# Kernel optimization log

Hardware: AMD Instinct MI355X
Metric: run time of the kernel (lower is better)

Reference implementation:

```python
import jax, jax.numpy as jnp
import numpy as np

N_NODES, D, H, L, E, N_DST = 100000, 64, 8, 3, 100000, 50000
HD = H * D
LEAKY_ALPHA = 0.01


def setup_inputs() -> dict:
    key = jax.random.key(0)
    ks = jax.random.split(key, 8)
    features = jax.random.normal(ks[0], (N_NODES, D), dtype=jnp.float32)
    edge_metapath_indices = jax.random.randint(ks[1], (E, L), 0, N_NODES)
    dst = jax.random.randint(ks[2], (E,), 0, N_DST)
    s = 1.0 / np.sqrt(HD)
    W_ih = jax.random.uniform(ks[3], (3 * HD, D), jnp.float32, -s, s)
    W_hh = jax.random.uniform(ks[4], (3 * HD, HD), jnp.float32, -s, s)
    b_ih = jax.random.uniform(ks[5], (3 * HD,), jnp.float32, -s, s)
    b_hh = jax.random.uniform(ks[6], (3 * HD,), jnp.float32, -s, s)
    attn = jax.random.normal(ks[7], (1, H, D), dtype=jnp.float32) * (1.414 / np.sqrt(D))
    return {"features": features, "W_ih": W_ih, "W_hh": W_hh, "b_ih": b_ih,
            "b_hh": b_hh, "attn": attn,
            "edge_metapath_indices": edge_metapath_indices, "dst": dst,
            "num_dst": N_DST}


def _gru_last_hidden(x_seq, W_ih, W_hh, b_ih, b_hh):
    # x_seq: [L, E, D]; torch nn.GRU gate math, return final hidden [E, HD]
    h0 = jnp.zeros((x_seq.shape[1], HD), dtype=x_seq.dtype)

    def step(h, x):
        gi = x @ W_ih.T + b_ih            # [E, 3HD]
        gh = h @ W_hh.T + b_hh            # [E, 3HD]
        i_r, i_z, i_n = jnp.split(gi, 3, axis=-1)
        h_r, h_z, h_n = jnp.split(gh, 3, axis=-1)
        r = jax.nn.sigmoid(i_r + h_r)
        z = jax.nn.sigmoid(i_z + h_z)
        n = jnp.tanh(i_n + r * h_n)
        h_new = (1.0 - z) * n + z * h
        return h_new, None

    h_last, _ = jax.lax.scan(step, h0, x_seq)
    return h_last


def reference(features, W_ih, W_hh, b_ih, b_hh, attn,
              edge_metapath_indices, dst, num_dst):
    # gather metapath node embeddings: [E, L, D]
    edata = features[edge_metapath_indices]
    # per-edge GRU over the metapath sequence -> final hidden [E, HD]
    hidden = _gru_last_hidden(jnp.transpose(edata, (1, 0, 2)), W_ih, W_hh, b_ih, b_hh)
    eft = hidden.reshape(-1, H, D)                         # [E, H, D]
    # attention logits per edge/head + leaky relu
    a = jnp.sum(eft * attn, axis=-1)                       # [E, H]
    a = jnp.where(a > 0, a, LEAKY_ALPHA * a)
    # edge softmax over destination-node segments (stable)
    a_max = jax.ops.segment_max(a, dst, num_segments=num_dst)    # [ND, H]
    a_exp = jnp.exp(a - a_max[dst])
    a_sum = jax.ops.segment_sum(a_exp, dst, num_segments=num_dst)
    alpha = a_exp / a_sum[dst]                             # [E, H]
    # scatter-sum aggregation of attention-weighted edge features
    ft = jax.ops.segment_sum(eft * alpha[:, :, None], dst, num_segments=num_dst)
    return ft                                              # [ND, H, D]
```

## Files before the change

### kernel.cpp

```cpp
#include <hip/hip_runtime.h>

typedef __attribute__((ext_vector_type(8))) short bf16x8;
typedef __attribute__((ext_vector_type(4))) float f32x4;

#define E_N   100000
#define ND_N  50000
#define NN_N  100000
#define SLOTS 32

__device__ __forceinline__ float b2f(unsigned short u) {
    return __uint_as_float(((unsigned int)u) << 16);
}
__device__ __forceinline__ unsigned short f2b(float f) {
    unsigned int b = __float_as_uint(f);
    b += 0x7fffu + ((b >> 16) & 1u);
    return (unsigned short)(b >> 16);
}
__device__ __forceinline__ float frcp(float x) { return __builtin_amdgcn_rcpf(x); }
__device__ __forceinline__ float fsig(float x) { return frcp(1.f + __expf(-x)); }
__device__ __forceinline__ float ftanhf(float x) {
    float e = __expf(2.f * x);
    return 1.f - 2.f * frcp(e + 1.f);
}

#define GLDS16(g, l)                                                        \
    __builtin_amdgcn_global_load_lds(                                       \
        (const __attribute__((address_space(1))) void*)(g),                 \
        (__attribute__((address_space(3))) void*)(l), 16, 0, 0)

__device__ __forceinline__ void wait_and_barrier() {
    __builtin_amdgcn_sched_barrier(0);
    asm volatile("s_waitcnt vmcnt(0)" ::: "memory");
    __builtin_amdgcn_s_barrier();
    __builtin_amdgcn_sched_barrier(0);
}
__device__ __forceinline__ void plain_barrier() {
    __builtin_amdgcn_sched_barrier(0);
    __builtin_amdgcn_s_barrier();
    __builtin_amdgcn_sched_barrier(0);
}

__global__ void conv_f2b(const float* __restrict__ src, unsigned short* __restrict__ dst, int n4) {
    int i = blockIdx.x * 256 + threadIdx.x;
    if (i < n4) {
        float4 v = ((const float4*)src)[i];
        ushort4 o;
        o.x = f2b(v.x); o.y = f2b(v.y); o.z = f2b(v.z); o.w = f2b(v.w);
        ((ushort4*)dst)[i] = o;
    }
}

__global__ void zero_u4(uint4* __restrict__ p, int n4) {
    int i = blockIdx.x * 256 + threadIdx.x;
    if (i < n4) p[i] = make_uint4(0u, 0u, 0u, 0u);
}

template<int G2>
__device__ __forceinline__ void mma_tile(
    const unsigned char* __restrict__ buf,
    f32x4 acc[4][2][2], int wm, int wn, int l15, int hi8)
{
    const unsigned char* lds_a = buf;
    const unsigned char* lds_b = buf + 16384;
    #pragma unroll
    for (int kk = 0; kk < 2; ++kk) {
        const int kb = kk * 64 + hi8 * 2;
        bf16x8 a[2];
        #pragma unroll
        for (int mi = 0; mi < 2; ++mi) {
            int row = wm * 32 + mi * 16 + l15;
            a[mi] = *(const bf16x8*)(lds_a + row * 128 + (kb ^ ((row & 7) << 4)));
        }
        #pragma unroll
        for (int g = 0; g < 3; ++g) {
            const int gi = (g == 2) ? G2 : g;
            bf16x8 b[2];
            #pragma unroll
            for (int ni = 0; ni < 2; ++ni) {
                int brow = g * 64 + wn * 32 + ni * 16 + l15;
                b[ni] = *(const bf16x8*)(lds_b + brow * 128 + (kb ^ ((brow & 7) << 4)));
            }
            #pragma unroll
            for (int mi = 0; mi < 2; ++mi)
                #pragma unroll
                for (int ni = 0; ni < 2; ++ni)
                    acc[gi][mi][ni] = __builtin_amdgcn_mfma_f32_16x16x32_bf16(
                        a[mi], b[ni], acc[gi][mi][ni], 0, 0, 0);
        }
    }
}

__global__ __launch_bounds__(512, 4) void gru_step(
    const unsigned short* __restrict__ feat16,
    const int* __restrict__ emi,
    const unsigned short* __restrict__ hprev,
    unsigned short* __restrict__ hnext,
    const unsigned short* __restrict__ wih,
    const unsigned short* __restrict__ whh,
    const float* __restrict__ bih,
    const float* __restrict__ bhh,
    int t)
{
    __shared__ __align__(16) unsigned char lds_mem[2 * 40960];

    const int tid = threadIdx.x;
    const int nwg = gridDim.x;
    const int logical = (blockIdx.x & 7) * (nwg >> 3) + (blockIdx.x >> 3);
    const int mb = (logical >> 3) * 128;
    const int nb = (logical & 7) * 64;
    const int hold_kt = nb >> 6;

    const int lane = tid & 63;
    const int wid  = tid >> 6;
    const int wm   = wid >> 1;
    const int wn   = wid & 1;
    const int l15  = lane & 15;
    const int hi8  = (lane >> 4) * 8;

    f32x4 acc[4][2][2];
    #pragma unroll
    for (int g = 0; g < 4; ++g)
        #pragma unroll
        for (int mi = 0; mi < 2; ++mi)
            #pragma unroll
            for (int ni = 0; ni < 2; ++ni) {
                f32x4 zz = {0.f, 0.f, 0.f, 0.f};
                acc[g][mi][ni] = zz;
            }

    int a_sl2[2], a_er[2];
    #pragma unroll
    for (int q = 0; q < 2; ++q) {
        int c = tid + q * 512;
        int row = c >> 3;
        a_sl2[q] = (c & 7) ^ (row & 7);
        int er = mb + row;
        a_er[q] = er < E_N ? er : E_N - 1;
    }
    int b_wr[3], b_sl2[3];
    #pragma unroll
    for (int q = 0; q < 3; ++q) {
        int c = tid + q * 512;
        int row = c >> 3;
        b_sl2[q] = (c & 7) ^ (row & 7);
        b_wr[q]  = (row >> 6) * 512 + nb + (row & 63);
    }

    #pragma unroll
    for (int q = 0; q < 2; ++q) {
        int node = emi[a_er[q] * 3 + t];
        GLDS16(feat16 + (size_t)node * 64 + a_sl2[q] * 8, lds_mem + (tid + q * 512) * 16);
    }
    #pragma unroll
    for (int q = 0; q < 3; ++q)
        GLDS16(wih + (size_t)b_wr[q] * 64 + b_sl2[q] * 8,
               lds_mem + 16384 + (tid + q * 512) * 16);
    if (t > 0) {
        #pragma unroll
        for (int q = 0; q < 2; ++q)
            GLDS16(hprev + (size_t)a_er[q] * 64 + a_sl2[q] * 8,
                   lds_mem + 40960 + (tid + q * 512) * 16);
        #pragma unroll
        for (int q = 0; q < 3; ++q)
            GLDS16(whh + (size_t)b_wr[q] * 512 + b_sl2[q] * 8,
                   lds_mem + 40960 + 16384 + (tid + q * 512) * 16);
    }
    wait_and_barrier();

    mma_tile<2>(lds_mem, acc, wm, wn, l15, hi8);
    plain_barrier();

    unsigned int holdp[2][2][2] = {{{0u,0u},{0u,0u}},{{0u,0u},{0u,0u}}};

    if (t > 0) {
        #pragma unroll
        for (int kt = 0; kt < 8; ++kt) {
            unsigned char*       wr = lds_mem + (kt & 1) * 40960;
            const unsigned char* rd = lds_mem + ((kt & 1) ^ 1) * 40960;
            if (kt < 7) {
                const size_t p1 = (size_t)(kt + 1) * E_N * 64;
                #pragma unroll
                for (int q = 0; q < 2; ++q)
                    GLDS16(hprev + p1 + (size_t)a_er[q] * 64 + a_sl2[q] * 8,
                           wr + (tid + q * 512) * 16);
                const int k1 = (kt + 1) * 64;
                #pragma unroll
                for (int q = 0; q < 3; ++q)
                    GLDS16(whh + (size_t)b_wr[q] * 512 + k1 + b_sl2[q] * 8,
                           wr + 16384 + (tid + q * 512) * 16);
            }
            if (kt == hold_kt) {
                #pragma unroll
                for (int ni = 0; ni < 2; ++ni)
                    #pragma unroll
                    for (int mi = 0; mi < 2; ++mi)
                        #pragma unroll
                        for (int jp = 0; jp < 2; ++jp) {
                            int r0 = wm * 32 + mi * 16 + (lane >> 4) * 4 + jp * 2;
                            int r1 = r0 + 1;
                            int ac = (wn * 32 + ni * 16 + l15) * 2;
                            unsigned int lo = *(const unsigned short*)(rd + r0 * 128 + (ac ^ ((r0 & 7) << 4)));
                            unsigned int hi = *(const unsigned short*)(rd + r1 * 128 + (ac ^ ((r1 & 7) << 4)));
                            holdp[ni][mi][jp] = lo | (hi << 16);
                        }
            }
            mma_tile<3>(rd, acc, wm, wn, l15, hi8);
            wait_and_barrier();
        }
    }

    unsigned char* lout = lds_mem;
    #pragma unroll
    for (int ni = 0; ni < 2; ++ni) {
        const int col = nb + wn * 32 + ni * 16 + l15;
        const float br0  = bih[col] + bhh[col];
        const float bz0  = bih[512 + col] + bhh[512 + col];
        const float bin_ = bih[1024 + col];
        const float bhn_ = bhh[1024 + col];
        #pragma unroll
        for (int mi = 0; mi < 2; ++mi) {
            #pragma unroll
            for (int j = 0; j < 4; ++j) {
                float r = fsig(acc[0][mi][ni][j] + br0);
                float z = fsig(acc[1][mi][ni][j] + bz0);
                float n = ftanhf(acc[2][mi][ni][j] + bin_ + r * (acc[3][mi][ni][j] + bhn_));
                float hold = (t > 0)
                    ? b2f((unsigned short)((holdp[ni][mi][j >> 1] >> ((j & 1) * 16)) & 0xffffu))
                    : 0.f;
                float hv = (1.f - z) * n + z * hold;
                int row = wm * 32 + mi * 16 + (lane >> 4) * 4 + j;
                int oc  = (wn * 32 + ni * 16 + l15) * 2;
                *(unsigned short*)(lout + row * 128 + (oc ^ ((row & 7) << 4))) = f2b(hv);
            }
        }
    }
    __syncthreads();
    const size_t oplane = (size_t)(nb >> 6) * E_N * 64;
    #pragma unroll
    for (int q = 0; q < 2; ++q) {
        int chunk = tid + q * 512;
        int row = chunk >> 3, c8 = chunk & 7;
        int grow = mb + row;
        if (grow < E_N) {
            uint4 v = *(const uint4*)(lout + row * 128 + ((c8 * 16) ^ ((row & 7) << 4)));
            *(uint4*)(hnext + oplane + (size_t)grow * 64 + c8 * 8) = v;
        }
    }
}

__global__ __launch_bounds__(256) void attn_logits(
    const unsigned short* __restrict__ hl, const float* __restrict__ attnw,
    float* __restrict__ a)
{
    int e = blockIdx.x * 4 + (threadIdx.x >> 6);
    int lane = threadIdx.x & 63;
    int h = lane >> 3;
    int c8 = lane & 7;
    uint4 v = *(const uint4*)(hl + (size_t)h * E_N * 64 + (size_t)e * 64 + c8 * 8);
    int dp = c8 * 8;
    float4 w0 = *(const float4*)(attnw + h * 64 + dp);
    float4 w1 = *(const float4*)(attnw + h * 64 + dp + 4);
    const unsigned short* u = (const unsigned short*)&v;
    float s = b2f(u[0]) * w0.x + b2f(u[1]) * w0.y + b2f(u[2]) * w0.z + b2f(u[3]) * w0.w
            + b2f(u[4]) * w1.x + b2f(u[5]) * w1.y + b2f(u[6]) * w1.z + b2f(u[7]) * w1.w;
    s += __shfl_xor(s, 1);
    s += __shfl_xor(s, 2);
    s += __shfl_xor(s, 4);
    if ((lane & 7) == 0)
        a[e * 8 + h] = s > 0.f ? s : 0.01f * s;
}

__global__ __launch_bounds__(256) void build_lists(
    const int* __restrict__ dstp, int* __restrict__ cnt, int* __restrict__ lists)
{
    int e = blockIdx.x * 256 + threadIdx.x;
    if (e < E_N) {
        int d = dstp[e];
        int slot = atomicAdd(&cnt[d], 1);
        if (slot < SLOTS) lists[(size_t)d * SLOTS + slot] = e;
    }
}

__global__ __launch_bounds__(256) void aggregate(
    const unsigned short* __restrict__ hl, const float* __restrict__ a,
    const int* __restrict__ lists, const int* __restrict__ cnt,
    float* __restrict__ out)
{
    int d = blockIdx.x * 4 + (threadIdx.x >> 6);
    int lane = threadIdx.x & 63;
    int n = cnt[d];
    n = n < SLOTS ? n : SLOTS;
    const int h = lane >> 3;
    const int c8 = lane & 7;
    const int* lst = lists + (size_t)d * SLOTS;
    const unsigned short* plane = hl + (size_t)h * E_N * 64;

    float m = -1e30f;
    for (int i = 0; i < n; ++i)
        m = fmaxf(m, a[lst[i] * 8 + h]);
    float s = 0.f;
    for (int i = 0; i < n; ++i)
        s += __expf(a[lst[i] * 8 + h] - m);
    float rs = frcp(s);

    float acc[8] = {0.f, 0.f, 0.f, 0.f, 0.f, 0.f, 0.f, 0.f};
    for (int i = 0; i < n; ++i) {
        int e = lst[i];
        float alpha = __expf(a[e * 8 + h] - m) * rs;
        uint4 v = *(const uint4*)(plane + (size_t)e * 64 + c8 * 8);
        const unsigned short* u = (const unsigned short*)&v;
        #pragma unroll
        for (int j = 0; j < 8; ++j)
            acc[j] += alpha * b2f(u[j]);
    }
    float4 o0 = {acc[0], acc[1], acc[2], acc[3]};
    float4 o1 = {acc[4], acc[5], acc[6], acc[7]};
    float* op = out + (size_t)d * 512 + lane * 8;
    *(float4*)op = o0;
    *(float4*)(op + 4) = o1;
}

extern "C" void kernel_launch(void* const* d_in, const int* in_sizes, int n_in,
                              void* d_out, int out_size, void* d_ws, size_t ws_size,
                              hipStream_t stream)
{
    const float* features = (const float*)d_in[0];
    const float* W_ih     = (const float*)d_in[1];
    const float* W_hh     = (const float*)d_in[2];
    const float* b_ih     = (const float*)d_in[3];
    const float* b_hh     = (const float*)d_in[4];
    const float* attnw    = (const float*)d_in[5];
    const int*   emi      = (const int*)d_in[6];
    const int*   dstp     = (const int*)d_in[7];

    char* ws = (char*)d_ws;
    size_t off = 0;
    auto alloc = [&](size_t bytes) -> void* {
        void* p = ws + off;
        off = (off + bytes + 255) & ~(size_t)255;
        return p;
    };
    unsigned short* feat16 = (unsigned short*)alloc((size_t)NN_N * 64 * 2);
    unsigned short* wih16  = (unsigned short*)alloc((size_t)1536 * 64 * 2);
    unsigned short* whh16  = (unsigned short*)alloc((size_t)1536 * 512 * 2);
    unsigned short* h0     = (unsigned short*)alloc((size_t)E_N * 512 * 2);
    unsigned short* h1     = (unsigned short*)alloc((size_t)E_N * 512 * 2);
    float*          abuf   = (float*)alloc((size_t)E_N * 8 * 4);
    int*            cnt    = (int*)alloc((size_t)ND_N * 4);
    int*            lists  = (int*)alloc((size_t)ND_N * SLOTS * 4);

    conv_f2b<<<(NN_N * 64 / 4 + 255) / 256, 256, 0, stream>>>(features, feat16, NN_N * 64 / 4);
    conv_f2b<<<(1536 * 64 / 4 + 255) / 256, 256, 0, stream>>>(W_ih, wih16, 1536 * 64 / 4);
    conv_f2b<<<(1536 * 512 / 4 + 255) / 256, 256, 0, stream>>>(W_hh, whh16, 1536 * 512 / 4);

    zero_u4<<<(ND_N / 4 + 255) / 256, 256, 0, stream>>>((uint4*)cnt, ND_N / 4);

    const int grid = ((E_N + 127) / 128) * 8;
    gru_step<<<grid, 512, 0, stream>>>(feat16, emi, nullptr, h0, wih16, whh16, b_ih, b_hh, 0);
    gru_step<<<grid, 512, 0, stream>>>(feat16, emi, h0, h1, wih16, whh16, b_ih, b_hh, 1);
    gru_step<<<grid, 512, 0, stream>>>(feat16, emi, h1, h0, wih16, whh16, b_ih, b_hh, 2);

    attn_logits<<<E_N / 4, 256, 0, stream>>>(h0, attnw, abuf);
    build_lists<<<(E_N + 255) / 256, 256, 0, stream>>>(dstp, cnt, lists);
    aggregate<<<ND_N / 4, 256, 0, stream>>>(h0, abuf, lists, cnt, (float*)d_out);
}
```

Before: 739.3 us.

## Load GRU A-operands (x and h) directly into registers instead of LDS

The gathered feature rows and previous-hidden tiles used as MFMA A-operands are now loaded straight from global memory into registers in MFMA fragment layout, double-buffered across k-steps. Only the weight tiles stay in LDS. This shrinks LDS per block from 80KB to 48KB, which could allow more resident blocks and removes the LDS write/read round trip for A. In exchange, global loads are redundantly repeated across the two wn waves, the hold values are read from global with scalar 2-byte loads, and vector register pressure goes up.

After: 947.4 us. 28.1% more time.

```diff
diff --git a/kernel.cpp b/kernel.cpp
--- a/kernel.cpp
+++ b/kernel.cpp
@@ -57,20 +57,12 @@
 
 template<int G2>
 __device__ __forceinline__ void mma_tile(
-    const unsigned char* __restrict__ buf,
-    f32x4 acc[4][2][2], int wm, int wn, int l15, int hi8)
-{
-    const unsigned char* lds_a = buf;
-    const unsigned char* lds_b = buf + 16384;
+    const unsigned char* __restrict__ lds_b, const bf16x8 a[2][2],
+    f32x4 acc[4][2][2], int wn, int l15, int hi8)
+{
     #pragma unroll
     for (int kk = 0; kk < 2; ++kk) {
         const int kb = kk * 64 + hi8 * 2;
-        bf16x8 a[2];
-        #pragma unroll
-        for (int mi = 0; mi < 2; ++mi) {
-            int row = wm * 32 + mi * 16 + l15;
-            a[mi] = *(const bf16x8*)(lds_a + row * 128 + (kb ^ ((row & 7) << 4)));
-        }
         #pragma unroll
         for (int g = 0; g < 3; ++g) {
             const int gi = (g == 2) ? G2 : g;
@@ -85,7 +77,7 @@
                 #pragma unroll
                 for (int ni = 0; ni < 2; ++ni)
                     acc[gi][mi][ni] = __builtin_amdgcn_mfma_f32_16x16x32_bf16(
-                        a[mi], b[ni], acc[gi][mi][ni], 0, 0, 0);
+                        a[mi][kk], b[ni], acc[gi][mi][ni], 0, 0, 0);
         }
     }
 }
@@ -101,7 +93,7 @@
     const float* __restrict__ bhh,
     int t)
 {
-    __shared__ __align__(16) unsigned char lds_mem[2 * 40960];
+    __shared__ __align__(16) unsigned char lds_mem[2 * 24576];
 
     const int tid = threadIdx.x;
     const int nwg = gridDim.x;
@@ -128,15 +120,6 @@
                 acc[g][mi][ni] = zz;
             }
 
-    int a_sl2[2], a_er[2];
-    #pragma unroll
-    for (int q = 0; q < 2; ++q) {
-        int c = tid + q * 512;
-        int row = c >> 3;
-        a_sl2[q] = (c & 7) ^ (row & 7);
-        int er = mb + row;
-        a_er[q] = er < E_N ? er : E_N - 1;
-    }
     int b_wr[3], b_sl2[3];
     #pragma unroll
     for (int q = 0; q < 3; ++q) {
@@ -146,28 +129,44 @@
         b_wr[q]  = (row >> 6) * 512 + nb + (row & 63);
     }
 
-    #pragma unroll
-    for (int q = 0; q < 2; ++q) {
-        int node = emi[a_er[q] * 3 + t];
-        GLDS16(feat16 + (size_t)node * 64 + a_sl2[q] * 8, lds_mem + (tid + q * 512) * 16);
-    }
+    int ar[2];
+    #pragma unroll
+    for (int mi = 0; mi < 2; ++mi) {
+        int r = mb + wm * 32 + mi * 16 + l15;
+        ar[mi] = r < E_N ? r : E_N - 1;
+    }
+
     #pragma unroll
     for (int q = 0; q < 3; ++q)
-        GLDS16(wih + (size_t)b_wr[q] * 64 + b_sl2[q] * 8,
-               lds_mem + 16384 + (tid + q * 512) * 16);
+        GLDS16(wih + (size_t)b_wr[q] * 64 + b_sl2[q] * 8, lds_mem + (tid + q * 512) * 16);
     if (t > 0) {
-        #pragma unroll
-        for (int q = 0; q < 2; ++q)
-            GLDS16(hprev + (size_t)a_er[q] * 64 + a_sl2[q] * 8,
-                   lds_mem + 40960 + (tid + q * 512) * 16);
         #pragma unroll
         for (int q = 0; q < 3; ++q)
             GLDS16(whh + (size_t)b_wr[q] * 512 + b_sl2[q] * 8,
-                   lds_mem + 40960 + 16384 + (tid + q * 512) * 16);
+                   lds_mem + 24576 + (tid + q * 512) * 16);
+    }
+
+    bf16x8 ax[2][2];
+    #pragma unroll
+    for (int mi = 0; mi < 2; ++mi) {
+        int node = emi[ar[mi] * 3 + t];
+        const unsigned short* p = feat16 + (size_t)node * 64 + hi8;
+        ax[mi][0] = *(const bf16x8*)p;
+        ax[mi][1] = *(const bf16x8*)(p + 32);
+    }
+
+    bf16x8 areg[2][2][2];
+    if (t > 0) {
+        #pragma unroll
+        for (int mi = 0; mi < 2; ++mi) {
+            const unsigned short* p = hprev + (size_t)ar[mi] * 64 + hi8;
+            areg[0][mi][0] = *(const bf16x8*)p;
+            areg[0][mi][1] = *(const bf16x8*)(p + 32);
+        }
     }
     wait_and_barrier();
 
-    mma_tile<2>(lds_mem, acc, wm, wn, l15, hi8);
+    mma_tile<2>(lds_mem, ax, acc, wn, l15, hi8);
     plain_barrier();
 
     unsigned int holdp[2][2][2] = {{{0u,0u},{0u,0u}},{{0u,0u},{0u,0u}}};
@@ -175,36 +174,41 @@
     if (t > 0) {
         #pragma unroll
         for (int kt = 0; kt < 8; ++kt) {
-            unsigned char*       wr = lds_mem + (kt & 1) * 40960;
-            const unsigned char* rd = lds_mem + ((kt & 1) ^ 1) * 40960;
+            unsigned char*       wr = lds_mem + (kt & 1) * 24576;
+            const unsigned char* rd = lds_mem + ((kt & 1) ^ 1) * 24576;
             if (kt < 7) {
-                const size_t p1 = (size_t)(kt + 1) * E_N * 64;
+                const unsigned short* plane = hprev + (size_t)(kt + 1) * E_N * 64;
                 #pragma unroll
-                for (int q = 0; q < 2; ++q)
-                    GLDS16(hprev + p1 + (size_t)a_er[q] * 64 + a_sl2[q] * 8,
-                           wr + (tid + q * 512) * 16);
+                for (int mi = 0; mi < 2; ++mi) {
+                    const unsigned short* p = plane + (size_t)ar[mi] * 64 + hi8;
+                    areg[(kt + 1) & 1][mi][0] = *(const bf16x8*)p;
+                    areg[(kt + 1) & 1][mi][1] = *(const bf16x8*)(p + 32);
+                }
                 const int k1 = (kt + 1) * 64;
                 #pragma unroll
                 for (int q = 0; q < 3; ++q)
                     GLDS16(whh + (size_t)b_wr[q] * 512 + k1 + b_sl2[q] * 8,
-                           wr + 16384 + (tid + q * 512) * 16);
+                           wr + (tid + q * 512) * 16);
             }
             if (kt == hold_kt) {
+                const unsigned short* hp = hprev + (size_t)kt * E_N * 64;
                 #pragma unroll
                 for (int ni = 0; ni < 2; ++ni)
                     #pragma unroll
                     for (int mi = 0; mi < 2; ++mi)
                         #pragma unroll
                         for (int jp = 0; jp < 2; ++jp) {
-                            int r0 = wm * 32 + mi * 16 + (lane >> 4) * 4 + jp * 2;
+                            int r0 = mb + wm * 32 + mi * 16 + (lane >> 4) * 4 + jp * 2;
                             int r1 = r0 + 1;
-                            int ac = (wn * 32 + ni * 16 + l15) * 2;
-                            unsigned int lo = *(const unsigned short*)(rd + r0 * 128 + (ac ^ ((r0 & 7) << 4)));
-                            unsigned int hi = *(const unsigned short*)(rd + r1 * 128 + (ac ^ ((r1 & 7) << 4)));
+                            r0 = r0 < E_N ? r0 : E_N - 1;
+                            r1 = r1 < E_N ? r1 : E_N - 1;
+                            int c = wn * 32 + ni * 16 + l15;
+                            unsigned int lo = hp[(size_t)r0 * 64 + c];
+                            unsigned int hi = hp[(size_t)r1 * 64 + c];
                             holdp[ni][mi][jp] = lo | (hi << 16);
                         }
             }
-            mma_tile<3>(rd, acc, wm, wn, l15, hi8);
+            mma_tile<3>(rd, areg[kt & 1], acc, wn, l15, hi8);
             wait_and_barrier();
         }
     }
```
